# Kernel tuning notes

Hardware: AMD Instinct MI355X
Metric: run time of the kernel (lower is better)

## Reference

```python
import jax, jax.numpy as jnp
import numpy as np

EMBED_DIM = 1024
NUM_HEADS = 16
HEAD_DIM = EMBED_DIM // NUM_HEADS


def setup_inputs() -> dict:
    key = jax.random.key(0)
    k1, k2, k3, k4, k5 = jax.random.split(key, 5)
    B, S, D = 1, 4096, EMBED_DIM
    scale = 0.02
    return {
        "input": jax.random.normal(k1, (B, S, D), dtype=jnp.float32),
        "Wqkv": jax.random.normal(k2, (D, 3 * D), dtype=jnp.float32) * scale,
        "bqkv": jax.random.normal(k3, (3 * D,), dtype=jnp.float32) * scale,
        "Wo": jax.random.normal(k4, (D, D), dtype=jnp.float32) * scale,
        "bo": jax.random.normal(k5, (D,), dtype=jnp.float32) * scale,
    }


def reference(input, Wqkv, bqkv, Wo, bo):
    B, S, D = input.shape
    H, Hd = NUM_HEADS, HEAD_DIM
    qkv = input @ Wqkv + bqkv                        # [B, S, 3D]
    qkv = qkv.reshape(B, S, 3, H, Hd)
    qkv = jnp.transpose(qkv, (2, 0, 3, 1, 4))        # [3, B, H, S, Hd]
    q, k, v = qkv[0], qkv[1], qkv[2]
    scores = jnp.einsum("bhsd,bhtd->bhst", q, k) / (Hd ** 0.5)  # [B,H,S,S]
    causal = jnp.tril(jnp.ones((S, S), dtype=bool))[None, None]
    scores = jnp.where(causal, scores, -jnp.inf)
    attn = jax.nn.softmax(scores, axis=-1)
    out = jnp.einsum("bhst,bhtd->bhsd", attn, v)     # [B,H,S,Hd]
    out = jnp.transpose(out, (0, 2, 1, 3)).reshape(B, S, D)
    return out @ Wo + bo
```

## Files before the change

### kernel.cpp

```cpp
#include <hip/hip_runtime.h>

typedef __bf16 bf16;
typedef __bf16 bf16x8 __attribute__((ext_vector_type(8)));
typedef float f32x4 __attribute__((ext_vector_type(4)));
typedef float f32x16 __attribute__((ext_vector_type(16)));

#define MFMA16(a, b, c) __builtin_amdgcn_mfma_f32_16x16x32_bf16((a), (b), (c), 0, 0, 0)
#define MFMA32(a, b, c) __builtin_amdgcn_mfma_f32_32x32x16_bf16((a), (b), (c), 0, 0, 0)

typedef const __attribute__((address_space(1))) uint32_t glb_u32;
typedef __attribute__((address_space(3))) uint32_t lds_u32;
#define GLOAD16(gp, lp) __builtin_amdgcn_global_load_lds((glb_u32*)(gp), (lds_u32*)(lp), 16, 0, 0)

__global__ __launch_bounds__(256) void k_convX(const float* __restrict__ in, bf16* __restrict__ out) {
    size_t i = ((size_t)blockIdx.x * 256 + threadIdx.x) * 8;
    float4 a = *(const float4*)(in + i);
    float4 b = *(const float4*)(in + i + 4);
    bf16 e[8];
    e[0] = (bf16)a.x; e[1] = (bf16)a.y; e[2] = (bf16)a.z; e[3] = (bf16)a.w;
    e[4] = (bf16)b.x; e[5] = (bf16)b.y; e[6] = (bf16)b.z; e[7] = (bf16)b.w;
    uint4 u; __builtin_memcpy(&u, e, 16);
    *(uint4*)(out + i) = u;
}

__global__ __launch_bounds__(256) void k_tconv(const float* __restrict__ in, bf16* __restrict__ out,
                                               int R, int C) {
    __shared__ float tile[64][65];
    int bx = blockIdx.x, by = blockIdx.y;
    int t = threadIdx.x;
    for (int i = 0; i < 16; ++i) {
        int e = i * 256 + t; int r = e >> 6, c = e & 63;
        tile[r][c] = in[(size_t)(by * 64 + r) * C + bx * 64 + c];
    }
    __syncthreads();
    for (int i = 0; i < 16; ++i) {
        int e = i * 256 + t; int r = e >> 6, c = e & 63;
        out[(size_t)(bx * 64 + r) * R + by * 64 + c] = (bf16)tile[c][r];
    }
}

__global__ __launch_bounds__(256) void k_kpack(const uint4* __restrict__ in, uint4* __restrict__ out) {
    int c = blockIdx.x * 256 + threadIdx.x;
    int h = c >> 15;
    int r = c & 32767;
    int tile = r >> 8, kst = (r >> 6) & 3, l = r & 63;
    int t = tile * 32 + (l & 31);
    int dc = kst * 2 + (l >> 5);
    out[c] = in[((size_t)h * 4096 + t) * 8 + dc];
}

__global__ __launch_bounds__(256) void k_vtrans(const bf16* __restrict__ V, uint4* __restrict__ Vfr) {
    __shared__ bf16 tl[64][68];
    int t0 = blockIdx.x * 64;
    int h = blockIdx.y;
    int t = threadIdx.x;
    const bf16* Vh = V + (size_t)h * 4096 * 64;
    #pragma unroll
    for (int i = 0; i < 2; ++i) {
        int c = i * 256 + t; int row = c >> 3, ch = c & 7;
        uint4 v = *(const uint4*)(Vh + (size_t)(t0 + row) * 64 + ch * 8);
        bf16 e[8]; __builtin_memcpy(e, &v, 16);
        #pragma unroll
        for (int j = 0; j < 8; ++j) tl[row][ch * 8 + j] = e[j];
    }
    __syncthreads();
    uint4* Vfh = Vfr + (size_t)h * 32768;
    #pragma unroll
    for (int i = 0; i < 2; ++i) {
        int c = i * 256 + t; int d = c >> 3, tch = c & 7;
        bf16 e[8];
        #pragma unroll
        for (int j = 0; j < 8; ++j) e[j] = tl[tch * 8 + j][d];
        uint4 u; __builtin_memcpy(&u, e, 16);
        int tile = blockIdx.x * 2 + (tch >> 2);
        int chunk = tile * 256 + ((d >> 5) * 2 + ((tch >> 1) & 1)) * 64 + (d & 31) + 32 * (tch & 1);
        Vfh[chunk] = u;
    }
}

__device__ __forceinline__ void gemm128_core(const bf16* __restrict__ A, const bf16* __restrict__ Bt,
                                             int r0, int c0, int Kd, char* As, char* Bs,
                                             f32x4 (&acc)[4][4]) {
    int t = threadIdx.x, l = t & 63, w = t >> 6;
    int g = l >> 4, li = l & 15;
    int wr = w >> 1, wc = w & 1;
    for (int k0 = 0; k0 < Kd; k0 += 64) {
        __syncthreads();
        #pragma unroll
        for (int i = 0; i < 4; ++i) {
            int slot = i * 256 + t;
            int row = slot >> 3;
            int ch  = (slot & 7) ^ (row & 7);
            int base = (i * 256 + w * 64) * 16;
            GLOAD16(A  + (size_t)(r0 + row) * Kd + k0 + ch * 8, As + base);
            GLOAD16(Bt + (size_t)(c0 + row) * Kd + k0 + ch * 8, Bs + base);
        }
        __syncthreads();
        __builtin_amdgcn_s_setprio(1);
        #pragma unroll
        for (int kk = 0; kk < 2; ++kk) {
            bf16x8 af[4], bfr[4];
            #pragma unroll
            for (int m = 0; m < 4; ++m) {
                int row = wr * 64 + m * 16 + li;
                af[m] = *(const bf16x8*)(As + ((row * 128 + kk * 64 + g * 16) ^ ((row & 7) << 4)));
            }
            #pragma unroll
            for (int n = 0; n < 4; ++n) {
                int row = wc * 64 + n * 16 + li;
                bfr[n] = *(const bf16x8*)(Bs + ((row * 128 + kk * 64 + g * 16) ^ ((row & 7) << 4)));
            }
            #pragma unroll
            for (int m = 0; m < 4; ++m)
                #pragma unroll
                for (int n = 0; n < 4; ++n)
                    acc[m][n] = MFMA16(af[m], bfr[n], acc[m][n]);
        }
        __builtin_amdgcn_s_setprio(0);
    }
}

__global__ __launch_bounds__(256) void k_gemm_qkv(const bf16* __restrict__ Xb, const bf16* __restrict__ WqkvT,
                                                  const float* __restrict__ bqkv,
                                                  bf16* __restrict__ Q, bf16* __restrict__ K,
                                                  bf16* __restrict__ V) {
    __shared__ __align__(16) char As[16384];
    __shared__ __align__(16) char Bs[16384];
    int r0 = blockIdx.y * 128, c0 = blockIdx.x * 128;
    f32x4 acc[4][4] = {};
    gemm128_core(Xb, WqkvT, r0, c0, 1024, As, Bs, acc);
    int t = threadIdx.x, l = t & 63, w = t >> 6;
    int g = l >> 4, li = l & 15;
    int wr = w >> 1, wc = w & 1;
    int colbase = c0 + wc * 64;
    int sec = colbase >> 10;
    int head = (colbase & 1023) >> 6;
    bf16* dst = (sec == 0) ? Q : (sec == 1) ? K : V;
    float scale = (sec == 0) ? 0.125f * 1.44269504f : 1.0f;
    #pragma unroll
    for (int m = 0; m < 4; ++m)
        #pragma unroll
        for (int n = 0; n < 4; ++n) {
            int hd = n * 16 + li;
            float bias = bqkv[colbase + hd];
            #pragma unroll
            for (int r = 0; r < 4; ++r) {
                int row = r0 + wr * 64 + m * 16 + g * 4 + r;
                dst[(size_t)(head * 4096 + row) * 64 + hd] = (bf16)((acc[m][n][r] + bias) * scale);
            }
        }
}

__global__ __launch_bounds__(256) void k_gemm_out(const bf16* __restrict__ Ob, const bf16* __restrict__ WoT,
                                                  const float* __restrict__ bo, float* __restrict__ out) {
    __shared__ __align__(16) char As[16384];
    __shared__ __align__(16) char Bs[16384];
    int r0 = blockIdx.y * 128, c0 = blockIdx.x * 128;
    f32x4 acc[4][4] = {};
    gemm128_core(Ob, WoT, r0, c0, 1024, As, Bs, acc);
    int t = threadIdx.x, l = t & 63, w = t >> 6;
    int g = l >> 4, li = l & 15;
    int wr = w >> 1, wc = w & 1;
    #pragma unroll
    for (int m = 0; m < 4; ++m)
        #pragma unroll
        for (int n = 0; n < 4; ++n) {
            int col = c0 + wc * 64 + n * 16 + li;
            float bias = bo[col];
            #pragma unroll
            for (int r = 0; r < 4; ++r) {
                int row = r0 + wr * 64 + m * 16 + g * 4 + r;
                out[(size_t)row * 1024 + col] = acc[m][n][r] + bias;
            }
        }
}

__device__ __forceinline__ unsigned pkbf(float a, float b) {
    bf16 h0 = (bf16)a, h1 = (bf16)b;
    unsigned short u0, u1;
    __builtin_memcpy(&u0, &h0, 2); __builtin_memcpy(&u1, &h1, 2);
    return (unsigned)u0 | ((unsigned)u1 << 16);
}

__global__ __launch_bounds__(128) void k_attn(const bf16* __restrict__ Q, const uint4* __restrict__ Kfr,
                                              const uint4* __restrict__ Vfr, bf16* __restrict__ O) {
    __shared__ float Op[32][64];
    __shared__ float Ml[2][32];
    int bid = blockIdx.x;
    int h = bid & 15;
    int u = bid >> 4;
    int jj = (u < 64) ? u : 191 - u;
    int w = threadIdx.x >> 6;
    int l = threadIdx.x & 63;
    int lc = l & 31, hi = l >> 5;
    int hi4 = hi * 4, hi8 = hi * 8;
    const bf16* Qh = Q + (size_t)h * 4096 * 64;
    const uint4* Kh = Kfr + (size_t)h * 32768;
    const uint4* Vh = Vfr + (size_t)h * 32768;
    int nt = jj + 1;
    int hA = (nt + 1) >> 1;
    int tb = w ? hA : 0;
    int te = w ? nt : hA;

    f32x16 oacc[2] = {};
    float m = -1e30f, lsum = 0.f;
    uint4 kA[4], vA[4], kB[4], vB[4];
    bf16x8 qf[4];
    #pragma unroll
    for (int kst = 0; kst < 4; ++kst)
        qf[kst] = *(const bf16x8*)(Qh + (size_t)(jj * 32 + lc) * 64 + kst * 16 + hi8);

    auto compute = [&](int tt, uint4 (&kf)[4], uint4 (&vf)[4]) {
        f32x16 sacc = {};
        #pragma unroll
        for (int kst = 0; kst < 4; ++kst) {
            bf16x8 kk; __builtin_memcpy(&kk, &kf[kst], 16);
            sacc = MFMA32(kk, qf[kst], sacc);
        }
        if (tt == jj) {
            #pragma unroll
            for (int r = 0; r < 16; ++r) {
                int tloc = (r & 3) + 8 * (r >> 2) + hi4;
                if (tloc > lc) sacc[r] = -1e30f;
            }
        }
        float t8[8];
        #pragma unroll
        for (int r = 0; r < 8; ++r) t8[r] = fmaxf(sacc[r], sacc[r + 8]);
        float t4a = fmaxf(fmaxf(t8[0], t8[1]), fmaxf(t8[2], t8[3]));
        float t4b = fmaxf(fmaxf(t8[4], t8[5]), fmaxf(t8[6], t8[7]));
        float pm = fmaxf(t4a, t4b);
        pm = fmaxf(pm, __shfl_xor(pm, 32));
        if (!__all(pm - m <= 8.0f)) {
            float mn = fmaxf(m, pm);
            float al = exp2f(m - mn);
            #pragma unroll
            for (int r = 0; r < 16; ++r) {
                int ql = (r & 3) + 8 * (r >> 2) + hi4;
                float alb = __shfl(al, ql);
                oacc[0][r] *= alb;
                oacc[1][r] *= alb;
            }
            lsum *= al;
            m = mn;
        }
        float pv[16];
        float rs = 0.f;
        #pragma unroll
        for (int r = 0; r < 16; ++r) { pv[r] = exp2f(sacc[r] - m); rs += pv[r]; }
        lsum += rs;
        #pragma unroll
        for (int ks = 0; ks < 2; ++ks) {
            int b = ks * 8;
            unsigned a0 = pkbf(pv[b + 0], pv[b + 1]), b0 = pkbf(pv[b + 4], pv[b + 5]);
            unsigned a1 = pkbf(pv[b + 2], pv[b + 3]), b1v = pkbf(pv[b + 6], pv[b + 7]);
            unsigned xa0 = (unsigned)__shfl_xor((int)a0, 32);
            unsigned xb0 = (unsigned)__shfl_xor((int)b0, 32);
            unsigned xa1 = (unsigned)__shfl_xor((int)a1, 32);
            unsigned xb1 = (unsigned)__shfl_xor((int)b1v, 32);
            unsigned wsq[4];
            wsq[0] = hi ? xb0 : a0;
            wsq[1] = hi ? xb1 : a1;
            wsq[2] = hi ? b0 : xa0;
            wsq[3] = hi ? b1v : xa1;
            bf16x8 pa; __builtin_memcpy(&pa, wsq, 16);
            #pragma unroll
            for (int jt = 0; jt < 2; ++jt) {
                bf16x8 vv; __builtin_memcpy(&vv, &vf[jt * 2 + ks], 16);
                oacc[jt] = MFMA32(pa, vv, oacc[jt]);
            }
        }
    };

    if (te > tb) {
        #pragma unroll
        for (int i = 0; i < 4; ++i) {
            kA[i] = Kh[(size_t)tb * 256 + i * 64 + l];
            vA[i] = Vh[(size_t)tb * 256 + i * 64 + l];
        }
        int i = tb;
        for (; i + 2 <= te; i += 2) {
            const uint4* Kn = Kh + (size_t)(i + 1) * 256;
            const uint4* Vn = Vh + (size_t)(i + 1) * 256;
            #pragma unroll
            for (int q = 0; q < 4; ++q) { kB[q] = Kn[q * 64 + l]; vB[q] = Vn[q * 64 + l]; }
            compute(i, kA, vA);
            if (i + 2 < te) {
                const uint4* K2 = Kh + (size_t)(i + 2) * 256;
                const uint4* V2 = Vh + (size_t)(i + 2) * 256;
                #pragma unroll
                for (int q = 0; q < 4; ++q) { kA[q] = K2[q * 64 + l]; vA[q] = V2[q * 64 + l]; }
            }
            compute(i + 1, kB, vB);
        }
        if ((te - tb) & 1) compute(te - 1, kA, vA);
    }
    lsum += __shfl_xor(lsum, 32);

    if (w == 1) {
        #pragma unroll
        for (int r = 0; r < 16; ++r) {
            int ql = (r & 3) + 8 * (r >> 2) + hi4;
            Op[ql][lc]      = oacc[0][r];
            Op[ql][32 + lc] = oacc[1][r];
        }
        if (hi == 0) { Ml[0][lc] = m; Ml[1][lc] = lsum; }
    }
    __syncthreads();
    if (w == 0) {
        float mo = Ml[0][lc], lo = Ml[1][lc];
        float mm = fmaxf(m, mo);
        float alr = exp2f(m - mm), alo = exp2f(mo - mm);
        float lf = lsum * alr + lo * alo;
        float inv = 1.0f / lf;
        float fr = alr * inv, fo = alo * inv;
        int q0 = jj * 32;
        #pragma unroll
        for (int r = 0; r < 16; ++r) {
            int ql = (r & 3) + 8 * (r >> 2) + hi4;
            float frb = __shfl(fr, ql), fob = __shfl(fo, ql);
            float o0 = oacc[0][r] * frb + Op[ql][lc]      * fob;
            float o1 = oacc[1][r] * frb + Op[ql][32 + lc] * fob;
            int row = q0 + ql;
            O[(size_t)row * 1024 + h * 64 + lc]      = (bf16)o0;
            O[(size_t)row * 1024 + h * 64 + 32 + lc] = (bf16)o1;
        }
    }
}

extern "C" void kernel_launch(void* const* d_in, const int* in_sizes, int n_in,
                              void* d_out, int out_size, void* d_ws, size_t ws_size,
                              hipStream_t stream) {
    const float* X    = (const float*)d_in[0];
    const float* Wqkv = (const float*)d_in[1];
    const float* bqkv = (const float*)d_in[2];
    const float* Wo   = (const float*)d_in[3];
    const float* bo   = (const float*)d_in[4];
    float* out = (float*)d_out;

    char* ws = (char*)d_ws;
    const size_t MB = 1024 * 1024;
    bf16*  Xb    = (bf16*)(ws);
    bf16*  WqkvT = (bf16*)(ws + 8  * MB);
    bf16*  WoT   = (bf16*)(ws + 14 * MB);
    bf16*  Qb    = (bf16*)(ws + 16 * MB);
    bf16*  Kb    = (bf16*)(ws + 24 * MB);
    bf16*  Vb    = (bf16*)(ws + 32 * MB);
    uint4* Kfr   = (uint4*)(ws + 40 * MB);
    uint4* Vfr   = (uint4*)(ws + 48 * MB);
    bf16*  Ob    = Xb;

    k_convX<<<2048, 256, 0, stream>>>(X, Xb);
    k_tconv<<<dim3(48, 16), 256, 0, stream>>>(Wqkv, WqkvT, 1024, 3072);
    k_tconv<<<dim3(16, 16), 256, 0, stream>>>(Wo, WoT, 1024, 1024);
    k_gemm_qkv<<<dim3(24, 32), 256, 0, stream>>>(Xb, WqkvT, bqkv, Qb, Kb, Vb);
    k_kpack<<<2048, 256, 0, stream>>>((const uint4*)Kb, Kfr);
    k_vtrans<<<dim3(64, 16), 256, 0, stream>>>(Vb, Vfr);
    k_attn<<<2048, 128, 0, stream>>>(Qb, Kfr, Vfr, Ob);
    k_gemm_out<<<dim3(8, 32), 256, 0, stream>>>(Ob, WoT, bo, out);
}
```

Baseline: 162.5 us.

## Split attention key range across four waves with tree merge of partials

The attention block grows from two to four waves, each handling a quarter of the causal key tiles. The partial softmax states are combined in a two-level tree through shared memory. Blocks are now scheduled longest-first (descending query tile) in place of the previous paired ordering. This is meant to shorten the per-block critical path and improve load balance, at the cost of more LDS traffic, extra barriers, and lower per-wave work on short rows.

```diff
diff --git a/kernel.cpp b/kernel.cpp
--- a/kernel.cpp
+++ b/kernel.cpp
@@ -182,14 +182,13 @@
     return (unsigned)u0 | ((unsigned)u1 << 16);
 }
 
-__global__ __launch_bounds__(128) void k_attn(const bf16* __restrict__ Q, const uint4* __restrict__ Kfr,
+__global__ __launch_bounds__(256) void k_attn(const bf16* __restrict__ Q, const uint4* __restrict__ Kfr,
                                               const uint4* __restrict__ Vfr, bf16* __restrict__ O) {
-    __shared__ float Op[32][64];
-    __shared__ float Ml[2][32];
+    __shared__ float Buf[2][32][64];
+    __shared__ float Ml[2][2][32];
     int bid = blockIdx.x;
     int h = bid & 15;
-    int u = bid >> 4;
-    int jj = (u < 64) ? u : 191 - u;
+    int jj = 127 - (bid >> 4);
     int w = threadIdx.x >> 6;
     int l = threadIdx.x & 63;
     int lc = l & 31, hi = l >> 5;
@@ -198,9 +197,8 @@
     const uint4* Kh = Kfr + (size_t)h * 32768;
     const uint4* Vh = Vfr + (size_t)h * 32768;
     int nt = jj + 1;
-    int hA = (nt + 1) >> 1;
-    int tb = w ? hA : 0;
-    int te = w ? nt : hA;
+    int tb = (w * nt) >> 2;
+    int te = ((w + 1) * nt) >> 2;
 
     f32x16 oacc[2] = {};
     float m = -1e30f, lsum = 0.f;
@@ -297,30 +295,57 @@
     }
     lsum += __shfl_xor(lsum, 32);
 
-    if (w == 1) {
+    if (w & 1) {
+        int b = w >> 1;
         #pragma unroll
         for (int r = 0; r < 16; ++r) {
             int ql = (r & 3) + 8 * (r >> 2) + hi4;
-            Op[ql][lc]      = oacc[0][r];
-            Op[ql][32 + lc] = oacc[1][r];
-        }
-        if (hi == 0) { Ml[0][lc] = m; Ml[1][lc] = lsum; }
+            Buf[b][ql][lc]      = oacc[0][r];
+            Buf[b][ql][32 + lc] = oacc[1][r];
+        }
+        if (hi == 0) { Ml[b][0][lc] = m; Ml[b][1][lc] = lsum; }
+    }
+    __syncthreads();
+    if (!(w & 1)) {
+        int b = w >> 1;
+        float mo = Ml[b][0][lc], lo = Ml[b][1][lc];
+        float mm = fmaxf(m, mo);
+        float ar = exp2f(m - mm), ao = exp2f(mo - mm);
+        lsum = lsum * ar + lo * ao;
+        m = mm;
+        #pragma unroll
+        for (int r = 0; r < 16; ++r) {
+            int ql = (r & 3) + 8 * (r >> 2) + hi4;
+            float arb = __shfl(ar, ql), aob = __shfl(ao, ql);
+            oacc[0][r] = oacc[0][r] * arb + Buf[b][ql][lc]      * aob;
+            oacc[1][r] = oacc[1][r] * arb + Buf[b][ql][32 + lc] * aob;
+        }
+    }
+    __syncthreads();
+    if (w == 2) {
+        #pragma unroll
+        for (int r = 0; r < 16; ++r) {
+            int ql = (r & 3) + 8 * (r >> 2) + hi4;
+            Buf[0][ql][lc]      = oacc[0][r];
+            Buf[0][ql][32 + lc] = oacc[1][r];
+        }
+        if (hi == 0) { Ml[0][0][lc] = m; Ml[0][1][lc] = lsum; }
     }
     __syncthreads();
     if (w == 0) {
-        float mo = Ml[0][lc], lo = Ml[1][lc];
+        float mo = Ml[0][0][lc], lo = Ml[0][1][lc];
         float mm = fmaxf(m, mo);
-        float alr = exp2f(m - mm), alo = exp2f(mo - mm);
-        float lf = lsum * alr + lo * alo;
+        float ar = exp2f(m - mm), ao = exp2f(mo - mm);
+        float lf = lsum * ar + lo * ao;
         float inv = 1.0f / lf;
-        float fr = alr * inv, fo = alo * inv;
+        float fr = ar * inv, fo = ao * inv;
         int q0 = jj * 32;
         #pragma unroll
         for (int r = 0; r < 16; ++r) {
             int ql = (r & 3) + 8 * (r >> 2) + hi4;
             float frb = __shfl(fr, ql), fob = __shfl(fo, ql);
-            float o0 = oacc[0][r] * frb + Op[ql][lc]      * fob;
-            float o1 = oacc[1][r] * frb + Op[ql][32 + lc] * fob;
+            float o0 = oacc[0][r] * frb + Buf[0][ql][lc]      * fob;
+            float o1 = oacc[1][r] * frb + Buf[0][ql][32 + lc] * fob;
             int row = q0 + ql;
             O[(size_t)row * 1024 + h * 64 + lc]      = (bf16)o0;
             O[(size_t)row * 1024 + h * 64 + 32 + lc] = (bf16)o1;
@@ -356,6 +381,6 @@
     k_gemm_qkv<<<dim3(24, 32), 256, 0, stream>>>(Xb, WqkvT, bqkv, Qb, Kb, Vb);
     k_kpack<<<2048, 256, 0, stream>>>((const uint4*)Kb, Kfr);
     k_vtrans<<<dim3(64, 16), 256, 0, stream>>>(Vb, Vfr);
-    k_attn<<<2048, 128, 0, stream>>>(Qb, Kfr, Vfr, Ob);
+    k_attn<<<2048, 256, 0, stream>>>(Qb, Kfr, Vfr, Ob);
     k_gemm_out<<<dim3(8, 32), 256, 0, stream>>>(Ob, WoT, bo, out);
 }
```

Result: slower. 167.3 us (+3.0%).

## Use permlane32_swap for P repack and raise priority around MFMAs

Applied to the files above, without the earlier changes.

Replaces the four cross-half __shfl_xor exchanges plus selects that repack the softmax probabilities with two permlane32_swap instructions. It also wraps the QK and PV MFMA groups in s_setprio so waves issuing matrix work get scheduling priority, and splits the max and sum reductions into shorter independent chains. The intent is to cut the permute and select overhead in the attention inner loop and to keep the matrix pipe busy. Correctness depends on the permlane32_swap lane semantics matching the old select pattern.

```diff
diff --git a/kernel.cpp b/kernel.cpp
--- a/kernel.cpp
+++ b/kernel.cpp
@@ -4,6 +4,7 @@
 typedef __bf16 bf16x8 __attribute__((ext_vector_type(8)));
 typedef float f32x4 __attribute__((ext_vector_type(4)));
 typedef float f32x16 __attribute__((ext_vector_type(16)));
+typedef unsigned u32x2 __attribute__((ext_vector_type(2)));
 
 #define MFMA16(a, b, c) __builtin_amdgcn_mfma_f32_16x16x32_bf16((a), (b), (c), 0, 0, 0)
 #define MFMA32(a, b, c) __builtin_amdgcn_mfma_f32_32x32x16_bf16((a), (b), (c), 0, 0, 0)
@@ -212,11 +213,13 @@
 
     auto compute = [&](int tt, uint4 (&kf)[4], uint4 (&vf)[4]) {
         f32x16 sacc = {};
+        __builtin_amdgcn_s_setprio(1);
         #pragma unroll
         for (int kst = 0; kst < 4; ++kst) {
             bf16x8 kk; __builtin_memcpy(&kk, &kf[kst], 16);
             sacc = MFMA32(kk, qf[kst], sacc);
         }
+        __builtin_amdgcn_s_setprio(0);
         if (tt == jj) {
             #pragma unroll
             for (int r = 0; r < 16; ++r) {
@@ -227,9 +230,10 @@
         float t8[8];
         #pragma unroll
         for (int r = 0; r < 8; ++r) t8[r] = fmaxf(sacc[r], sacc[r + 8]);
-        float t4a = fmaxf(fmaxf(t8[0], t8[1]), fmaxf(t8[2], t8[3]));
-        float t4b = fmaxf(fmaxf(t8[4], t8[5]), fmaxf(t8[6], t8[7]));
-        float pm = fmaxf(t4a, t4b);
+        float ta = fmaxf(fmaxf(t8[0], t8[1]), t8[2]);
+        float tb3 = fmaxf(fmaxf(t8[3], t8[4]), t8[5]);
+        float tc = fmaxf(t8[6], t8[7]);
+        float pm = fmaxf(fmaxf(ta, tb3), tc);
         pm = fmaxf(pm, __shfl_xor(pm, 32));
         if (!__all(pm - m <= 8.0f)) {
             float mn = fmaxf(m, pm);
@@ -245,30 +249,29 @@
             m = mn;
         }
         float pv[16];
-        float rs = 0.f;
-        #pragma unroll
-        for (int r = 0; r < 16; ++r) { pv[r] = exp2f(sacc[r] - m); rs += pv[r]; }
-        lsum += rs;
+        float rs0 = 0.f, rs1 = 0.f;
+        #pragma unroll
+        for (int r = 0; r < 8; ++r) {
+            pv[r]     = exp2f(sacc[r] - m);     rs0 += pv[r];
+            pv[r + 8] = exp2f(sacc[r + 8] - m); rs1 += pv[r + 8];
+        }
+        lsum += rs0 + rs1;
         #pragma unroll
         for (int ks = 0; ks < 2; ++ks) {
             int b = ks * 8;
-            unsigned a0 = pkbf(pv[b + 0], pv[b + 1]), b0 = pkbf(pv[b + 4], pv[b + 5]);
-            unsigned a1 = pkbf(pv[b + 2], pv[b + 3]), b1v = pkbf(pv[b + 6], pv[b + 7]);
-            unsigned xa0 = (unsigned)__shfl_xor((int)a0, 32);
-            unsigned xb0 = (unsigned)__shfl_xor((int)b0, 32);
-            unsigned xa1 = (unsigned)__shfl_xor((int)a1, 32);
-            unsigned xb1 = (unsigned)__shfl_xor((int)b1v, 32);
-            unsigned wsq[4];
-            wsq[0] = hi ? xb0 : a0;
-            wsq[1] = hi ? xb1 : a1;
-            wsq[2] = hi ? b0 : xa0;
-            wsq[3] = hi ? b1v : xa1;
+            unsigned a0 = pkbf(pv[b + 0], pv[b + 1]), a1 = pkbf(pv[b + 2], pv[b + 3]);
+            unsigned b0 = pkbf(pv[b + 4], pv[b + 5]), b1 = pkbf(pv[b + 6], pv[b + 7]);
+            u32x2 r0 = __builtin_amdgcn_permlane32_swap(a0, b0, false, false);
+            u32x2 r1 = __builtin_amdgcn_permlane32_swap(a1, b1, false, false);
+            unsigned wsq[4] = { r0[0], r1[0], r0[1], r1[1] };
             bf16x8 pa; __builtin_memcpy(&pa, wsq, 16);
+            __builtin_amdgcn_s_setprio(1);
             #pragma unroll
             for (int jt = 0; jt < 2; ++jt) {
                 bf16x8 vv; __builtin_memcpy(&vv, &vf[jt * 2 + ks], 16);
                 oacc[jt] = MFMA32(pa, vv, oacc[jt]);
             }
+            __builtin_amdgcn_s_setprio(0);
         }
     };
 
```

Result: no change. 161.5 us (-0.6%).
